# Optimization experiments

Measured on AMD Instinct MI355X. Metric: run time of the kernel, lower is better.

Reference implementation:

```python
import jax, jax.numpy as jnp
import numpy as np

T, B, I, H = 512, 512, 128, 512

def setup_inputs() -> dict:
    key = jax.random.key(0)
    ks = jax.random.split(key, 10)
    s = 0.05  # small init scale to avoid gate saturation
    return {
        "x": jax.random.normal(ks[0], (T, B, I), jnp.float32),
        "enc_hiddens": jax.random.normal(ks[1], (1, B, H), jnp.float32),
        "h0": jax.random.normal(ks[2], (1, B, H), jnp.float32) * s,
        "c0": jax.random.normal(ks[3], (1, B, H), jnp.float32) * s,
        "W_ih": jax.random.normal(ks[4], (4 * H, I), jnp.float32) * s,
        "W_hh": jax.random.normal(ks[5], (4 * H, H), jnp.float32) * s,
        "b_ih": jax.random.normal(ks[6], (4 * H,), jnp.float32) * s,
        "b_hh": jax.random.normal(ks[7], (4 * H,), jnp.float32) * s,
        "fc_W": jax.random.normal(ks[8], (I, H), jnp.float32) * s,
        "fc_b": jax.random.normal(ks[9], (I,), jnp.float32) * s,
    }

def reference(x, enc_hiddens, h0, c0, W_ih, W_hh, b_ih, b_hh, fc_W, fc_b):
    # RECURSIVE decoding branch: feed own output back in; store outputs reversed.
    seq_len = x.shape[0]
    b = b_ih + b_hh  # fuse biases

    def step(carry, _):
        inp, h, c = carry  # inp:[B,I], h,c:[B,H]
        gates = inp @ W_ih.T + h @ W_hh.T + b  # [B,4H]
        i_g, f_g, g_g, o_g = jnp.split(gates, 4, axis=-1)  # torch gate order i,f,g,o
        i_g = jax.nn.sigmoid(i_g)
        f_g = jax.nn.sigmoid(f_g)
        g_g = jnp.tanh(g_g)
        o_g = jax.nn.sigmoid(o_g)
        c_new = f_g * c + i_g * g_g
        h_new = o_g * jnp.tanh(c_new)
        out = h_new @ fc_W.T + fc_b            # Linear
        out = 2.0 * jax.nn.sigmoid(out) - 1.0  # use_act affine rescale
        return (out, h_new, c_new), out

    init = (x[seq_len - 1], h0[0], c0[0])
    _, outs = jax.lax.scan(step, init, None, length=seq_len)  # [T,B,I], step t stored at index t
    # original writes dec_outs[seq_len - t - 1], i.e. reversed order
    return jnp.flip(outs, axis=0)
```

## Files before the change

kernel.cpp:

```cpp
#include <hip/hip_runtime.h>

typedef unsigned short u16;
typedef unsigned int   u32;
typedef unsigned long long u64;
typedef short v8s __attribute__((ext_vector_type(8)));
typedef float v16f __attribute__((ext_vector_type(16)));
typedef float v2f  __attribute__((ext_vector_type(2)));

#define B_ 512
#define I_ 128
#define H_ 512
#define KK 640
#define NSTEP 512
#define AST 648

__device__ inline u16 f2b(float x){
  union{float f; unsigned u;} v; v.f = x;
  unsigned r = v.u + 0x7fffu + ((v.u >> 16) & 1u);
  return (u16)(r >> 16);
}

__device__ inline float tanh_fast(float x){
  float e = __expf(2.f * x);
  return 1.f - 2.f / (e + 1.f);
}

__device__ inline u64 ld64(const u16* p){
  return __hip_atomic_load((const u64*)p, __ATOMIC_RELAXED, __HIP_MEMORY_SCOPE_AGENT);
}
__device__ inline void st32(u16* p, u32 v){
  __hip_atomic_store((u32*)p, v, __ATOMIC_RELAXED, __HIP_MEMORY_SCOPE_AGENT);
}
__device__ inline u32 fpoll(const u32* p){
  return __hip_atomic_load(p, __ATOMIC_RELAXED, __HIP_MEMORY_SCOPE_AGENT);
}
__device__ inline void fst(u32* p, u32 v){
  __hip_atomic_store(p, v, __ATOMIC_RELAXED, __HIP_MEMORY_SCOPE_AGENT);
}

__global__ void init_kernel(const float* __restrict__ x, const float* __restrict__ h0,
    const float* __restrict__ Wih, const float* __restrict__ Whh,
    const float* __restrict__ bih, const float* __restrict__ bhh, const float* __restrict__ fcW,
    u16* __restrict__ Wcat, u16* __restrict__ fcWb, float* __restrict__ bsum,
    u16* __restrict__ hb0, u16* __restrict__ outb, u32* __restrict__ flags)
{
  int idx = blockIdx.x * 256 + threadIdx.x;
  if (idx < 1310720) {
    int g = idx / 640, k = idx - g * 640;
    float v = (k < 512) ? Whh[g * 512 + k] : Wih[g * 128 + (k - 512)];
    Wcat[idx] = f2b(v);
  } else if (idx < 1376256) {
    int i = idx - 1310720; fcWb[i] = f2b(fcW[i]);
  } else if (idx < 1378304) {
    int i = idx - 1376256; bsum[i] = bih[i] + bhh[i];
  } else if (idx < 1640448) {
    int i = idx - 1378304; hb0[i] = f2b(h0[i]);
  } else if (idx < 1705984) {
    int i = idx - 1640448; outb[i] = f2b(x[33488896 + i]);
  } else if (idx < 1706240) {
    flags[idx - 1705984] = 0u;
  }
}

__global__ __launch_bounds__(512, 2) void decoder_persist(
    const u16* __restrict__ Wcat, const float* __restrict__ bsum,
    const u16* __restrict__ fcWb, const float* __restrict__ fcb,
    const float* __restrict__ c0,
    u16* __restrict__ hb0, u16* __restrict__ hb1, const u16* __restrict__ outb,
    float* __restrict__ dout, u32* __restrict__ flags)
{
  __shared__ __align__(16) u16  Alds[32 * AST];
  __shared__ __align__(16) float gbuf[4096];

  const int tid  = threadIdx.x;
  const int wid  = tid >> 6, lane = tid & 63;
  const int l31  = lane & 31, q2 = lane >> 5;
  const int mb   = blockIdx.x & 15;
  const int nb   = blockIdx.x >> 4;
  const int R    = mb * 32;
  u32* hf = flags + mb * 16;

  const bool isfc = (wid >= 4);
  const int  wc   = (wid - 4) * 32;

  v8s wfrag[40];
  if (!isfc) {
    const u16* wr = Wcat + (u64)(wid * 512 + nb * 32 + l31) * KK + q2 * 8;
    #pragma unroll
    for (int kc = 0; kc < 40; ++kc) wfrag[kc] = *reinterpret_cast<const v8s*>(wr + kc * 16);
  } else {
    const u16* fr = fcWb + (u64)(wc + l31) * H_ + q2 * 8;
    #pragma unroll
    for (int kc = 0; kc < 32; ++kc) wfrag[kc] = *reinterpret_cast<const v8s*>(fr + kc * 16);
    #pragma unroll
    for (int kc = 32; kc < 40; ++kc) wfrag[kc] = (v8s){0,0,0,0,0,0,0,0};
  }
  const float bias0 = isfc ? fcb[wc + l31] : bsum[wid * 512 + nb * 32 + l31];

  const bool dopred = isfc && (((wc + l31) >> 3) == nb);

  const int crow = tid >> 4, ccol = (tid * 2) & 31;
  float cv0 = c0[(R + crow) * H_ + nb * 32 + ccol];
  float cv1 = c0[(R + crow) * H_ + nb * 32 + ccol + 1];

  for (int t = 0; t <= NSTEP; ++t) {
    const u16* hsrc = (t & 1) ? hb1 : hb0;

    if (t > 0 && wid == 0 && lane < 16) {
      while (fpoll(hf + lane) < (u32)t) {}
    }
    __asm__ volatile("" ::: "memory");
    __syncthreads();

    {
      u64 tmp[8];
      #pragma unroll
      for (int u = 0; u < 8; ++u) {
        int v = u * 512 + tid;
        int row = v >> 7, cc = v & 127;
        tmp[u] = ld64(hsrc + (R + row) * H_ + cc * 4);
      }
      #pragma unroll
      for (int u = 0; u < 8; ++u) {
        int v = u * 512 + tid;
        int row = v >> 7, cc = v & 127;
        *reinterpret_cast<u64*>(&Alds[row * AST + cc * 4]) = tmp[u];
      }
    }
    if (t == 0) {
      u64 tmp[2];
      #pragma unroll
      for (int u = 0; u < 2; ++u) {
        int v = u * 512 + tid;
        int row = v >> 5, cc = v & 31;
        tmp[u] = ld64(outb + (R + row) * I_ + cc * 4);
      }
      #pragma unroll
      for (int u = 0; u < 2; ++u) {
        int v = u * 512 + tid;
        int row = v >> 5, cc = v & 31;
        *reinterpret_cast<u64*>(&Alds[row * AST + 512 + cc * 4]) = tmp[u];
      }
    }
    __syncthreads();

    v16f acc = {0.f,0.f,0.f,0.f,0.f,0.f,0.f,0.f,0.f,0.f,0.f,0.f,0.f,0.f,0.f,0.f};
    const u16* abase = &Alds[l31 * AST + q2 * 8];
    #pragma unroll
    for (int kc = 0; kc < 32; ++kc) {
      v8s a = *reinterpret_cast<const v8s*>(abase + kc * 16);
      acc = __builtin_amdgcn_mfma_f32_32x32x16_bf16(a, wfrag[kc], acc, 0, 0, 0);
    }

    if (isfc && t > 0) {
      float* dt = dout + (u64)(NSTEP - t) * (B_ * I_) + wc + l31;
      #pragma unroll
      for (int r = 0; r < 16; ++r) {
        int row = (r & 3) + 8 * (r >> 2) + 4 * q2;
        float o = 2.f / (1.f + __expf(-(acc[r] + bias0))) - 1.f;
        Alds[row * AST + 512 + wc + l31] = f2b(o);
        if (dopred) __builtin_nontemporal_store(o, dt + (R + row) * I_);
      }
    }
    __syncthreads();

    if (t < NSTEP) {
      if (!isfc) {
        #pragma unroll
        for (int kc = 32; kc < 40; ++kc) {
          v8s a = *reinterpret_cast<const v8s*>(abase + kc * 16);
          acc = __builtin_amdgcn_mfma_f32_32x32x16_bf16(a, wfrag[kc], acc, 0, 0, 0);
        }
        #pragma unroll
        for (int r = 0; r < 16; ++r) {
          int row = (r & 3) + 8 * (r >> 2) + 4 * q2;
          float z = acc[r] + bias0;
          float a2 = (wid == 2) ? tanh_fast(z) : 1.f / (1.f + __expf(-z));
          gbuf[wid * 1024 + row * 32 + l31] = a2;
        }
      }
      __syncthreads();

      u16* hdst = (t & 1) ? hb0 : hb1;
      v2f ig = *reinterpret_cast<const v2f*>(&gbuf[       crow * 32 + ccol]);
      v2f fg = *reinterpret_cast<const v2f*>(&gbuf[1024 + crow * 32 + ccol]);
      v2f gg = *reinterpret_cast<const v2f*>(&gbuf[2048 + crow * 32 + ccol]);
      v2f og = *reinterpret_cast<const v2f*>(&gbuf[3072 + crow * 32 + ccol]);
      float cn0 = fg[0] * cv0 + ig[0] * gg[0];
      float cn1 = fg[1] * cv1 + ig[1] * gg[1];
      cv0 = cn0; cv1 = cn1;
      u32 packed = (u32)f2b(og[0] * tanh_fast(cn0)) | ((u32)f2b(og[1] * tanh_fast(cn1)) << 16);
      st32(hdst + (R + crow) * H_ + nb * 32 + ccol, packed);
      __syncthreads();
      __asm__ volatile("" ::: "memory");
      if (tid == 0) fst(hf + nb, (u32)(t + 1));
    }
  }
}

extern "C" void kernel_launch(void* const* d_in, const int* in_sizes, int n_in,
                              void* d_out, int out_size, void* d_ws, size_t ws_size,
                              hipStream_t stream)
{
  const float* x   = (const float*)d_in[0];
  const float* h0  = (const float*)d_in[2];
  const float* c0  = (const float*)d_in[3];
  const float* Wih = (const float*)d_in[4];
  const float* Whh = (const float*)d_in[5];
  const float* bih = (const float*)d_in[6];
  const float* bhh = (const float*)d_in[7];
  const float* fcW = (const float*)d_in[8];
  const float* fcb = (const float*)d_in[9];

  char* p = (char*)d_ws;
  u16*   Wcat  = (u16*)p;   p += 2048LL * 640 * 2;
  u16*   fcWb  = (u16*)p;   p += 128 * 512 * 2;
  float* bsum  = (float*)p; p += 2048 * 4;
  u16*   hb0   = (u16*)p;   p += 512 * 512 * 2;
  u16*   hb1   = (u16*)p;   p += 512 * 512 * 2;
  u16*   outb  = (u16*)p;   p += 512 * 128 * 2;
  u32*   flags = (u32*)p;   p += 256 * 4;
  float* dout  = (float*)d_out;

  init_kernel<<<6666, 256, 0, stream>>>(x, h0, Wih, Whh, bih, bhh, fcW,
                                        Wcat, fcWb, bsum, hb0, outb, flags);
  decoder_persist<<<256, 512, 0, stream>>>(Wcat, bsum, fcWb, fcb, c0,
                                           hb0, hb1, outb, dout, flags);
}
```

Baseline: 3.071 ms.

## Merge FC and gate warps into four warps per block with per-warp flag polling

Shrinks the persistent block from 8 waves to 4. Each wave now computes both its gate tile and its FC output tile, issuing two interleaved MFMA chains over the same A fragment. Every wave polls its own subset of flags with a wave-wide vote and loads its own column slice of h into LDS, so the single-wave spin followed by a block barrier is gone. The aim is to shorten the per-step critical path by removing the serialized FC phase and one barrier, at the cost of more registers per lane (72 weight fragments) and fewer waves to hide latency.

```diff
diff --git a/kernel.cpp b/kernel.cpp
--- a/kernel.cpp
+++ b/kernel.cpp
@@ -62,7 +62,7 @@
   }
 }
 
-__global__ __launch_bounds__(512, 2) void decoder_persist(
+__global__ __launch_bounds__(256, 1) void decoder_persist(
     const u16* __restrict__ Wcat, const float* __restrict__ bsum,
     const u16* __restrict__ fcWb, const float* __restrict__ fcb,
     const float* __restrict__ c0,
@@ -80,121 +80,134 @@
   const int R    = mb * 32;
   u32* hf = flags + mb * 16;
 
-  const bool isfc = (wid >= 4);
-  const int  wc   = (wid - 4) * 32;
-
-  v8s wfrag[40];
-  if (!isfc) {
+  v8s wfg[40];
+  {
     const u16* wr = Wcat + (u64)(wid * 512 + nb * 32 + l31) * KK + q2 * 8;
     #pragma unroll
-    for (int kc = 0; kc < 40; ++kc) wfrag[kc] = *reinterpret_cast<const v8s*>(wr + kc * 16);
-  } else {
-    const u16* fr = fcWb + (u64)(wc + l31) * H_ + q2 * 8;
+    for (int kc = 0; kc < 40; ++kc) wfg[kc] = *reinterpret_cast<const v8s*>(wr + kc * 16);
+  }
+  v8s wff[32];
+  {
+    const u16* fr = fcWb + (u64)(wid * 32 + l31) * H_ + q2 * 8;
     #pragma unroll
-    for (int kc = 0; kc < 32; ++kc) wfrag[kc] = *reinterpret_cast<const v8s*>(fr + kc * 16);
-    #pragma unroll
-    for (int kc = 32; kc < 40; ++kc) wfrag[kc] = (v8s){0,0,0,0,0,0,0,0};
-  }
-  const float bias0 = isfc ? fcb[wc + l31] : bsum[wid * 512 + nb * 32 + l31];
-
-  const bool dopred = isfc && (((wc + l31) >> 3) == nb);
-
-  const int crow = tid >> 4, ccol = (tid * 2) & 31;
-  float cv0 = c0[(R + crow) * H_ + nb * 32 + ccol];
-  float cv1 = c0[(R + crow) * H_ + nb * 32 + ccol + 1];
+    for (int kc = 0; kc < 32; ++kc) wff[kc] = *reinterpret_cast<const v8s*>(fr + kc * 16);
+  }
+
+  const float bg = bsum[wid * 512 + nb * 32 + l31];
+  const float bf = fcb[wid * 32 + l31];
+  const int  fccol = wid * 32 + l31;
+  const bool dopred = ((fccol >> 3) == nb);
+
+  const int crow0 = tid >> 4, ccol = (tid & 15) * 2;
+  float cv[4];
+  #pragma unroll
+  for (int p = 0; p < 2; ++p) {
+    int row = p * 16 + crow0;
+    cv[2*p]   = c0[(R + row) * H_ + nb * 32 + ccol];
+    cv[2*p+1] = c0[(R + row) * H_ + nb * 32 + ccol + 1];
+  }
+
+  const u16* hsrc = hb0;
+  u16*       hdst = hb1;
 
   for (int t = 0; t <= NSTEP; ++t) {
-    const u16* hsrc = (t & 1) ? hb1 : hb0;
-
-    if (t > 0 && wid == 0 && lane < 16) {
-      while (fpoll(hf + lane) < (u32)t) {}
-    }
-    __asm__ volatile("" ::: "memory");
+    if (t > 0) {
+      const u32 tt = (u32)t;
+      for (;;) {
+        u32 f = fpoll(hf + wid * 4 + (lane & 3));
+        if (__all((int)(f >= tt))) break;
+      }
+      __asm__ volatile("" ::: "memory");
+    }
+    {
+      u64 tmp[16];
+      #pragma unroll
+      for (int k = 0; k < 16; ++k) {
+        int v = k * 64 + lane;
+        int row = v >> 5, c = v & 31;
+        tmp[k] = ld64(hsrc + (R + row) * H_ + wid * 128 + c * 4);
+      }
+      #pragma unroll
+      for (int k = 0; k < 16; ++k) {
+        int v = k * 64 + lane;
+        int row = v >> 5, c = v & 31;
+        *reinterpret_cast<u64*>(&Alds[row * AST + wid * 128 + c * 4]) = tmp[k];
+      }
+    }
+    if (t == 0) {
+      u64 tmp[4];
+      #pragma unroll
+      for (int k = 0; k < 4; ++k) {
+        int v = k * 256 + tid;
+        int row = v >> 5, c = v & 31;
+        tmp[k] = ld64(outb + (R + row) * I_ + c * 4);
+      }
+      #pragma unroll
+      for (int k = 0; k < 4; ++k) {
+        int v = k * 256 + tid;
+        int row = v >> 5, c = v & 31;
+        *reinterpret_cast<u64*>(&Alds[row * AST + 512 + c * 4]) = tmp[k];
+      }
+    }
     __syncthreads();
 
-    {
-      u64 tmp[8];
-      #pragma unroll
-      for (int u = 0; u < 8; ++u) {
-        int v = u * 512 + tid;
-        int row = v >> 7, cc = v & 127;
-        tmp[u] = ld64(hsrc + (R + row) * H_ + cc * 4);
-      }
-      #pragma unroll
-      for (int u = 0; u < 8; ++u) {
-        int v = u * 512 + tid;
-        int row = v >> 7, cc = v & 127;
-        *reinterpret_cast<u64*>(&Alds[row * AST + cc * 4]) = tmp[u];
-      }
-    }
-    if (t == 0) {
-      u64 tmp[2];
-      #pragma unroll
-      for (int u = 0; u < 2; ++u) {
-        int v = u * 512 + tid;
-        int row = v >> 5, cc = v & 31;
-        tmp[u] = ld64(outb + (R + row) * I_ + cc * 4);
-      }
-      #pragma unroll
-      for (int u = 0; u < 2; ++u) {
-        int v = u * 512 + tid;
-        int row = v >> 5, cc = v & 31;
-        *reinterpret_cast<u64*>(&Alds[row * AST + 512 + cc * 4]) = tmp[u];
-      }
-    }
-    __syncthreads();
-
-    v16f acc = {0.f,0.f,0.f,0.f,0.f,0.f,0.f,0.f,0.f,0.f,0.f,0.f,0.f,0.f,0.f,0.f};
-    const u16* abase = &Alds[l31 * AST + q2 * 8];
+    v16f accg = {0.f,0.f,0.f,0.f,0.f,0.f,0.f,0.f,0.f,0.f,0.f,0.f,0.f,0.f,0.f,0.f};
+    v16f accf = {0.f,0.f,0.f,0.f,0.f,0.f,0.f,0.f,0.f,0.f,0.f,0.f,0.f,0.f,0.f,0.f};
+    const u16* ab = &Alds[l31 * AST + q2 * 8];
     #pragma unroll
     for (int kc = 0; kc < 32; ++kc) {
-      v8s a = *reinterpret_cast<const v8s*>(abase + kc * 16);
-      acc = __builtin_amdgcn_mfma_f32_32x32x16_bf16(a, wfrag[kc], acc, 0, 0, 0);
-    }
-
-    if (isfc && t > 0) {
-      float* dt = dout + (u64)(NSTEP - t) * (B_ * I_) + wc + l31;
+      v8s a = *reinterpret_cast<const v8s*>(ab + kc * 16);
+      accg = __builtin_amdgcn_mfma_f32_32x32x16_bf16(a, wfg[kc], accg, 0, 0, 0);
+      accf = __builtin_amdgcn_mfma_f32_32x32x16_bf16(a, wff[kc], accf, 0, 0, 0);
+    }
+
+    if (t > 0) {
+      float* dt = dout + (u64)(NSTEP - t) * (B_ * I_);
       #pragma unroll
       for (int r = 0; r < 16; ++r) {
         int row = (r & 3) + 8 * (r >> 2) + 4 * q2;
-        float o = 2.f / (1.f + __expf(-(acc[r] + bias0))) - 1.f;
-        Alds[row * AST + 512 + wc + l31] = f2b(o);
-        if (dopred) __builtin_nontemporal_store(o, dt + (R + row) * I_);
+        float o = 2.f / (1.f + __expf(-(accf[r] + bf))) - 1.f;
+        Alds[row * AST + 512 + fccol] = f2b(o);
+        if (dopred) __builtin_nontemporal_store(o, dt + (R + row) * I_ + fccol);
       }
     }
     __syncthreads();
 
     if (t < NSTEP) {
-      if (!isfc) {
-        #pragma unroll
-        for (int kc = 32; kc < 40; ++kc) {
-          v8s a = *reinterpret_cast<const v8s*>(abase + kc * 16);
-          acc = __builtin_amdgcn_mfma_f32_32x32x16_bf16(a, wfrag[kc], acc, 0, 0, 0);
-        }
-        #pragma unroll
-        for (int r = 0; r < 16; ++r) {
-          int row = (r & 3) + 8 * (r >> 2) + 4 * q2;
-          float z = acc[r] + bias0;
-          float a2 = (wid == 2) ? tanh_fast(z) : 1.f / (1.f + __expf(-z));
-          gbuf[wid * 1024 + row * 32 + l31] = a2;
-        }
+      #pragma unroll
+      for (int kc = 32; kc < 40; ++kc) {
+        v8s a = *reinterpret_cast<const v8s*>(ab + kc * 16);
+        accg = __builtin_amdgcn_mfma_f32_32x32x16_bf16(a, wfg[kc], accg, 0, 0, 0);
+      }
+      #pragma unroll
+      for (int r = 0; r < 16; ++r) {
+        int row = (r & 3) + 8 * (r >> 2) + 4 * q2;
+        float z = accg[r] + bg;
+        float a2 = (wid == 2) ? tanh_fast(z) : 1.f / (1.f + __expf(-z));
+        gbuf[wid * 1024 + row * 32 + l31] = a2;
       }
       __syncthreads();
 
-      u16* hdst = (t & 1) ? hb0 : hb1;
-      v2f ig = *reinterpret_cast<const v2f*>(&gbuf[       crow * 32 + ccol]);
-      v2f fg = *reinterpret_cast<const v2f*>(&gbuf[1024 + crow * 32 + ccol]);
-      v2f gg = *reinterpret_cast<const v2f*>(&gbuf[2048 + crow * 32 + ccol]);
-      v2f og = *reinterpret_cast<const v2f*>(&gbuf[3072 + crow * 32 + ccol]);
-      float cn0 = fg[0] * cv0 + ig[0] * gg[0];
-      float cn1 = fg[1] * cv1 + ig[1] * gg[1];
-      cv0 = cn0; cv1 = cn1;
-      u32 packed = (u32)f2b(og[0] * tanh_fast(cn0)) | ((u32)f2b(og[1] * tanh_fast(cn1)) << 16);
-      st32(hdst + (R + crow) * H_ + nb * 32 + ccol, packed);
+      #pragma unroll
+      for (int p = 0; p < 2; ++p) {
+        int row = p * 16 + crow0;
+        int base = row * 32 + ccol;
+        v2f ig = *reinterpret_cast<const v2f*>(&gbuf[       base]);
+        v2f fg = *reinterpret_cast<const v2f*>(&gbuf[1024 + base]);
+        v2f gg = *reinterpret_cast<const v2f*>(&gbuf[2048 + base]);
+        v2f og = *reinterpret_cast<const v2f*>(&gbuf[3072 + base]);
+        float cn0 = fg[0] * cv[2*p]   + ig[0] * gg[0];
+        float cn1 = fg[1] * cv[2*p+1] + ig[1] * gg[1];
+        cv[2*p] = cn0; cv[2*p+1] = cn1;
+        u32 packed = (u32)f2b(og[0] * tanh_fast(cn0)) | ((u32)f2b(og[1] * tanh_fast(cn1)) << 16);
+        st32(hdst + (R + row) * H_ + nb * 32 + ccol, packed);
+      }
       __syncthreads();
       __asm__ volatile("" ::: "memory");
       if (tid == 0) fst(hf + nb, (u32)(t + 1));
     }
+
+    { const u16* tp = hsrc; hsrc = hdst; hdst = (u16*)tp; }
   }
 }
 
@@ -224,6 +237,6 @@
 
   init_kernel<<<6666, 256, 0, stream>>>(x, h0, Wih, Whh, bih, bhh, fcW,
                                         Wcat, fcWb, bsum, hb0, outb, flags);
-  decoder_persist<<<256, 512, 0, stream>>>(Wcat, bsum, fcWb, fcb, c0,
+  decoder_persist<<<256, 256, 0, stream>>>(Wcat, bsum, fcWb, fcb, c0,
                                            hb0, hb1, outb, dout, flags);
 }
```

Measured after the change: 3.285 ms. 6.9% more time.

## Poll flags per-wave, split h loads by wave column, defer output stores

Applied to the files above, without the earlier changes.

Each wave now polls only the two producer flags for the 64-column slice of h it loads, then loads that slice itself. This replaces the single-wave poll followed by a block-wide barrier, so waves can start loading as soon as their own producers finish. Output stores from the fc waves are buffered in registers and issued at the start of the next step, taking them off the critical path. s_setprio raises priority around the MFMA loops. The risk is extra polling traffic from all eight waves and higher register pressure from holding the buffered outputs.

```diff
diff --git a/kernel.cpp b/kernel.cpp
--- a/kernel.cpp
+++ b/kernel.cpp
@@ -99,6 +99,9 @@
 
   const bool dopred = isfc && (((wc + l31) >> 3) == nb);
 
+  float oreg[16];
+  float* dpend = nullptr;
+
   const int crow = tid >> 4, ccol = (tid * 2) & 31;
   float cv0 = c0[(R + crow) * H_ + nb * 32 + ccol];
   float cv1 = c0[(R + crow) * H_ + nb * 32 + ccol + 1];
@@ -106,25 +109,37 @@
   for (int t = 0; t <= NSTEP; ++t) {
     const u16* hsrc = (t & 1) ? hb1 : hb0;
 
-    if (t > 0 && wid == 0 && lane < 16) {
-      while (fpoll(hf + lane) < (u32)t) {}
-    }
-    __asm__ volatile("" ::: "memory");
-    __syncthreads();
+    if (dopred && dpend) {
+      #pragma unroll
+      for (int r = 0; r < 16; ++r) {
+        int row = (r & 3) + 8 * (r >> 2) + 4 * q2;
+        __builtin_nontemporal_store(oreg[r], dpend + (R + row) * I_ + wc + l31);
+      }
+      dpend = nullptr;
+    }
+
+    if (t > 0) {
+      const u32 tt = (u32)t;
+      for (;;) {
+        u32 f = fpoll(hf + 2 * wid + (lane & 1));
+        if (__all((int)(f >= tt))) break;
+      }
+      __asm__ volatile("" ::: "memory");
+    }
 
     {
       u64 tmp[8];
       #pragma unroll
-      for (int u = 0; u < 8; ++u) {
-        int v = u * 512 + tid;
-        int row = v >> 7, cc = v & 127;
-        tmp[u] = ld64(hsrc + (R + row) * H_ + cc * 4);
-      }
-      #pragma unroll
-      for (int u = 0; u < 8; ++u) {
-        int v = u * 512 + tid;
-        int row = v >> 7, cc = v & 127;
-        *reinterpret_cast<u64*>(&Alds[row * AST + cc * 4]) = tmp[u];
+      for (int k = 0; k < 8; ++k) {
+        int v = k * 64 + lane;
+        int row = v >> 4, c16 = v & 15;
+        tmp[k] = ld64(hsrc + (R + row) * H_ + wid * 64 + c16 * 4);
+      }
+      #pragma unroll
+      for (int k = 0; k < 8; ++k) {
+        int v = k * 64 + lane;
+        int row = v >> 4, c16 = v & 15;
+        *reinterpret_cast<u64*>(&Alds[row * AST + wid * 64 + c16 * 4]) = tmp[k];
       }
     }
     if (t == 0) {
@@ -145,32 +160,36 @@
     __syncthreads();
 
     v16f acc = {0.f,0.f,0.f,0.f,0.f,0.f,0.f,0.f,0.f,0.f,0.f,0.f,0.f,0.f,0.f,0.f};
-    const u16* abase = &Alds[l31 * AST + q2 * 8];
+    const u16* ab = &Alds[l31 * AST + q2 * 8];
+    __builtin_amdgcn_s_setprio(1);
     #pragma unroll
     for (int kc = 0; kc < 32; ++kc) {
-      v8s a = *reinterpret_cast<const v8s*>(abase + kc * 16);
+      v8s a = *reinterpret_cast<const v8s*>(ab + kc * 16);
       acc = __builtin_amdgcn_mfma_f32_32x32x16_bf16(a, wfrag[kc], acc, 0, 0, 0);
     }
+    __builtin_amdgcn_s_setprio(0);
 
     if (isfc && t > 0) {
-      float* dt = dout + (u64)(NSTEP - t) * (B_ * I_) + wc + l31;
       #pragma unroll
       for (int r = 0; r < 16; ++r) {
         int row = (r & 3) + 8 * (r >> 2) + 4 * q2;
         float o = 2.f / (1.f + __expf(-(acc[r] + bias0))) - 1.f;
+        oreg[r] = o;
         Alds[row * AST + 512 + wc + l31] = f2b(o);
-        if (dopred) __builtin_nontemporal_store(o, dt + (R + row) * I_);
-      }
+      }
+      dpend = dout + (u64)(NSTEP - t) * (B_ * I_);
     }
     __syncthreads();
 
     if (t < NSTEP) {
       if (!isfc) {
+        __builtin_amdgcn_s_setprio(1);
         #pragma unroll
         for (int kc = 32; kc < 40; ++kc) {
-          v8s a = *reinterpret_cast<const v8s*>(abase + kc * 16);
+          v8s a = *reinterpret_cast<const v8s*>(ab + kc * 16);
           acc = __builtin_amdgcn_mfma_f32_32x32x16_bf16(a, wfrag[kc], acc, 0, 0, 0);
         }
+        __builtin_amdgcn_s_setprio(0);
         #pragma unroll
         for (int r = 0; r < 16; ++r) {
           int row = (r & 3) + 8 * (r >> 2) + 4 * q2;
@@ -196,6 +215,14 @@
       if (tid == 0) fst(hf + nb, (u32)(t + 1));
     }
   }
+
+  if (dopred && dpend) {
+    #pragma unroll
+    for (int r = 0; r < 16; ++r) {
+      int row = (r & 3) + 8 * (r >> 2) + 4 * q2;
+      __builtin_nontemporal_store(oreg[r], dpend + (R + row) * I_ + wc + l31);
+    }
+  }
 }
 
 extern "C" void kernel_launch(void* const* d_in, const int* in_sizes, int n_in,
```

After: 2.770 ms. -9.8%, faster.
